# Performance work log

Hardware: AMD Instinct MI355X
Metric: run time of the kernel (lower is better)

The kernel has to match this reference:

```python
import jax, jax.numpy as jnp
import numpy as np
import math

B, T, D, H = 2, 2048, 1024, 16
DK = D // H
NEG = -1e9  # finite stand-in for -inf causal fill inside the ALiBi bias


def make_alibi_bias(n_heads: int, seq_len: int) -> jnp.ndarray:
    # standard ALiBi slopes: 2^(-8*h/H) for h = 1..H
    slopes = 2.0 ** (-8.0 * (np.arange(1, n_heads + 1) / n_heads))  # [H]
    pos = np.arange(seq_len)
    dist = pos[None, :] - pos[:, None]  # [T,T], j - i
    bias = slopes[:, None, None] * dist[None, :, :]  # [H,T,T], <=0 below diag
    bias = np.where(dist[None] > 0, NEG, bias)  # causal: mask future
    return jnp.asarray(bias, dtype=jnp.float32)


def setup_inputs() -> dict:
    key = jax.random.key(0)
    ks = jax.random.split(key, 8)
    s = 0.02
    return {
        "query": jax.random.normal(ks[0], (B, T, D), jnp.float32),
        "key": jax.random.normal(ks[1], (B, T, D), jnp.float32),
        "value": jax.random.normal(ks[2], (B, T, D), jnp.float32),
        "alibi_bias": make_alibi_bias(H, T),
        "wq": jax.random.normal(ks[3], (D, D), jnp.float32) * s,
        "wk": jax.random.normal(ks[4], (D, D), jnp.float32) * s,
        "wv": jax.random.normal(ks[5], (D, D), jnp.float32) * s,
        "wo": jax.random.normal(ks[6], (D, D), jnp.float32) * s,
        "bo": jnp.zeros((D,), jnp.float32),
    }


def reference(query, key, value, alibi_bias, wq, wk, wv, wo, bo):
    b, tq, d = query.shape
    # linear projections (torch Linear: x @ W^T), split heads -> [B,H,T,d_k]
    def split(x, w):
        y = jnp.einsum('btd,ed->bte', x, w)
        return y.reshape(b, -1, H, DK).transpose(0, 2, 1, 3)
    Q, K, V = split(query, wq), split(key, wk), split(value, wv)
    # scores + ALiBi bias (bias already encodes causality)
    scores = jnp.einsum('bhqd,bhkd->bhqk', Q, K) / math.sqrt(DK)
    scores = scores + alibi_bias[None]  # broadcast over batch
    attn = jax.nn.softmax(scores, axis=-1)
    out = jnp.einsum('bhqk,bhkd->bhqd', attn, V)  # [B,H,Tq,d_k]
    out = out.transpose(0, 2, 1, 3).reshape(b, tq, d)
    return jnp.einsum('btd,ed->bte', out, wo) + bo
```

## Files before the change

kernel.cpp:

```cpp
#include <hip/hip_runtime.h>
#include <hip/hip_bf16.h>
#include <stdint.h>

#define Bc   2
#define Tc   2048
#define Dc   1024
#define Hc   16
#define DKc  64
#define BTc  4096
#define LOG2E 1.44269504088896f

typedef unsigned short u16;
typedef unsigned int u32;
typedef __attribute__((ext_vector_type(8))) short bf16x8;
typedef __attribute__((ext_vector_type(4))) float f32x4;
typedef __attribute__((ext_vector_type(2))) u32 u32x2;

static __device__ __forceinline__ u16 f2bf(float f) {
  union { float f; unsigned u; } v; v.f = f;
  unsigned r = v.u + 0x7fffu + ((v.u >> 16) & 1u);
  return (u16)(r >> 16);
}

static __device__ __forceinline__ u32 cvt_pk_bf16(float lo, float hi) {
  u32 r;
  asm volatile("v_cvt_pk_bf16_f32 %0, %1, %2" : "=v"(r) : "v"(lo), "v"(hi));
  return r;
}

static __device__ __forceinline__ f32x4 mfma16(bf16x8 a, bf16x8 b, f32x4 c) {
  return __builtin_amdgcn_mfma_f32_16x16x32_bf16(a, b, c, 0, 0, 0);
}

__global__ void conv_kernel(const float* __restrict__ q, const float* __restrict__ k,
                            const float* __restrict__ v, const float* __restrict__ wq,
                            const float* __restrict__ wk, const float* __restrict__ wv,
                            const float* __restrict__ wo,
                            u16* __restrict__ Xq, u16* __restrict__ Xk, u16* __restrict__ Xv,
                            u16* __restrict__ Wq, u16* __restrict__ Wk, u16* __restrict__ Wv,
                            u16* __restrict__ Wo) {
  int z = blockIdx.z, bx = blockIdx.x;
  const float* src; u16* dst; int i;
  if (bx < 4096) {
    if (z == 3) return;
    src = z == 0 ? q : z == 1 ? k : v;
    dst = z == 0 ? Xq : z == 1 ? Xk : Xv;
    i = bx * 256 + threadIdx.x;
  } else {
    src = z == 0 ? wq : z == 1 ? wk : z == 2 ? wv : wo;
    dst = z == 0 ? Wq : z == 1 ? Wk : z == 2 ? Wv : Wo;
    i = (bx - 4096) * 256 + threadIdx.x;
  }
  float4 f = ((const float4*)src)[i];
  ushort4 r; r.x = f2bf(f.x); r.y = f2bf(f.y); r.z = f2bf(f.z); r.w = f2bf(f.w);
  ((ushort4*)dst)[i] = r;
}

#define AS1 const __attribute__((address_space(1))) void*
#define AS3 __attribute__((address_space(3))) void*

__global__ __launch_bounds__(256) void gemm_proj(const u16* __restrict__ Xq, const u16* __restrict__ Xk,
                                                 const u16* __restrict__ Xv, const u16* __restrict__ Wq,
                                                 const u16* __restrict__ Wk, const u16* __restrict__ Wv,
                                                 u16* __restrict__ Qh, u16* __restrict__ Kh,
                                                 u16* __restrict__ VTo) {
  __shared__ u16 As[128 * 32];
  __shared__ u16 Bs[128 * 32];
  int z = blockIdx.z;
  const u16* A = z == 0 ? Xq : z == 1 ? Xk : Xv;
  const u16* W = z == 0 ? Wq : z == 1 ? Wk : Wv;
  u16* outp    = z == 0 ? Qh : z == 1 ? Kh : VTo;
  float scale = (z == 0) ? 0.125f * LOG2E : 1.0f;
  int tid = threadIdx.x;
  int lane = tid & 63, wave = tid >> 6;
  int ln = lane & 15, g = lane >> 4;
  int m0 = blockIdx.x * 128, n0 = blockIdx.y * 128;
  int wm = (wave >> 1) * 64, wn = (wave & 1) * 64;
  f32x4 acc[4][4] = {};
  int c0 = tid, c1 = tid + 256;
  const u16* gA0 = A + (size_t)(m0 + (c0 >> 2)) * 1024 + (c0 & 3) * 8;
  const u16* gA1 = A + (size_t)(m0 + (c1 >> 2)) * 1024 + (c1 & 3) * 8;
  const u16* gW0 = W + (size_t)(n0 + (c0 >> 2)) * 1024 + (c0 & 3) * 8;
  const u16* gW1 = W + (size_t)(n0 + (c1 >> 2)) * 1024 + (c1 & 3) * 8;
  for (int k0 = 0; k0 < 1024; k0 += 32) {
    __builtin_amdgcn_global_load_lds((AS1)(gA0 + k0), (AS3)(As + c0 * 8), 16, 0, 0);
    __builtin_amdgcn_global_load_lds((AS1)(gA1 + k0), (AS3)(As + c1 * 8), 16, 0, 0);
    __builtin_amdgcn_global_load_lds((AS1)(gW0 + k0), (AS3)(Bs + c0 * 8), 16, 0, 0);
    __builtin_amdgcn_global_load_lds((AS1)(gW1 + k0), (AS3)(Bs + c1 * 8), 16, 0, 0);
    __syncthreads();
    bf16x8 af[4], bfr[4];
#pragma unroll
    for (int mi = 0; mi < 4; ++mi) af[mi]  = *(const bf16x8*)&As[(wm + mi * 16 + ln) * 32 + g * 8];
#pragma unroll
    for (int ni = 0; ni < 4; ++ni) bfr[ni] = *(const bf16x8*)&Bs[(wn + ni * 16 + ln) * 32 + g * 8];
#pragma unroll
    for (int mi = 0; mi < 4; ++mi)
#pragma unroll
      for (int ni = 0; ni < 4; ++ni)
        acc[mi][ni] = mfma16(af[mi], bfr[ni], acc[mi][ni]);
    __syncthreads();
  }
  if (z == 2) {
#pragma unroll
    for (int mi = 0; mi < 4; ++mi)
#pragma unroll
      for (int ni = 0; ni < 4; ++ni) {
        int t0 = m0 + wm + mi * 16 + g * 4;
        int gn = n0 + wn + ni * 16 + ln;
        size_t bhead = ((size_t)(t0 >> 11)) * Hc + (gn >> 6);
        ushort4 pk;
        pk.x = f2bf(acc[mi][ni][0]); pk.y = f2bf(acc[mi][ni][1]);
        pk.z = f2bf(acc[mi][ni][2]); pk.w = f2bf(acc[mi][ni][3]);
        *(ushort4*)&outp[(bhead * DKc + (gn & 63)) * Tc + (t0 & 2047)] = pk;
      }
  } else {
#pragma unroll
    for (int mi = 0; mi < 4; ++mi)
#pragma unroll
      for (int ni = 0; ni < 4; ++ni)
#pragma unroll
        for (int r = 0; r < 4; ++r) {
          int gm = m0 + wm + mi * 16 + g * 4 + r;
          int gn = n0 + wn + ni * 16 + ln;
          size_t bhead = ((size_t)(gm >> 11)) * Hc + (gn >> 6);
          outp[(bhead * Tc + (gm & 2047)) * DKc + (gn & 63)] = f2bf(acc[mi][ni][r] * scale);
        }
  }
}

__global__ __launch_bounds__(256) void gemm_out(const u16* __restrict__ Ain, const u16* __restrict__ W,
                                                float* __restrict__ of, const float* __restrict__ bias) {
  __shared__ u16 As[64 * 32];
  __shared__ u16 Bs[128 * 32];
  int tid = threadIdx.x;
  int lane = tid & 63, wave = tid >> 6;
  int ln = lane & 15, g = lane >> 4;
  int m0 = blockIdx.x * 64, n0 = blockIdx.y * 128;
  int wm = (wave >> 1) * 32, wn = (wave & 1) * 64;
  f32x4 acc[2][4] = {};
  int ca = tid, cb0 = tid, cb1 = tid + 256;
  const u16* gA  = Ain + (size_t)(m0 + (ca  >> 2)) * 1024 + (ca  & 3) * 8;
  const u16* gW0 = W   + (size_t)(n0 + (cb0 >> 2)) * 1024 + (cb0 & 3) * 8;
  const u16* gW1 = W   + (size_t)(n0 + (cb1 >> 2)) * 1024 + (cb1 & 3) * 8;
  for (int k0 = 0; k0 < 1024; k0 += 32) {
    __builtin_amdgcn_global_load_lds((AS1)(gA  + k0), (AS3)(As + ca  * 8), 16, 0, 0);
    __builtin_amdgcn_global_load_lds((AS1)(gW0 + k0), (AS3)(Bs + cb0 * 8), 16, 0, 0);
    __builtin_amdgcn_global_load_lds((AS1)(gW1 + k0), (AS3)(Bs + cb1 * 8), 16, 0, 0);
    __syncthreads();
    bf16x8 af[2], bfr[4];
#pragma unroll
    for (int mi = 0; mi < 2; ++mi) af[mi]  = *(const bf16x8*)&As[(wm + mi * 16 + ln) * 32 + g * 8];
#pragma unroll
    for (int ni = 0; ni < 4; ++ni) bfr[ni] = *(const bf16x8*)&Bs[(wn + ni * 16 + ln) * 32 + g * 8];
#pragma unroll
    for (int mi = 0; mi < 2; ++mi)
#pragma unroll
      for (int ni = 0; ni < 4; ++ni)
        acc[mi][ni] = mfma16(af[mi], bfr[ni], acc[mi][ni]);
    __syncthreads();
  }
#pragma unroll
  for (int mi = 0; mi < 2; ++mi)
#pragma unroll
    for (int ni = 0; ni < 4; ++ni)
#pragma unroll
      for (int r = 0; r < 4; ++r) {
        int gm = m0 + wm + mi * 16 + g * 4 + r;
        int gn = n0 + wn + ni * 16 + ln;
        of[(size_t)gm * 1024 + gn] = acc[mi][ni][r] + bias[gn];
      }
}

__global__ __launch_bounds__(256, 2) void flash_attn(const u16* __restrict__ Qh,
                                                     const u16* __restrict__ Kh,
                                                     const u16* __restrict__ VT,
                                                     u16* __restrict__ O) {
  __shared__ u16 Ks[2][64 * 64];
  __shared__ u16 Vs[2][64 * 64];
  __shared__ u16 P_lds[8][16][64];
  int d = blockIdx.x;
  int logical = (d & 7) * 64 + (d >> 3);
  int bh = logical >> 4, pid = logical & 15;
  int qhi = 16 + pid, qlo = 15 - pid;
  int b = bh >> 4, h = bh & (Hc - 1);
  int tid = threadIdx.x, wave = tid >> 6, lane = tid & 63;
  int ln = lane & 15, g = lane >> 4;
  float slope2 = exp2f(-0.5f * (float)(h + 1)) * LOG2E;

  const u16* gK = Kh + (size_t)bh * Tc * DKc;
  const u16* gV = VT + (size_t)bh * DKc * Tc;
  int c0 = tid, c1 = tid + 256;
  int r0 = c0 >> 3, r1 = c1 >> 3;
  int e0 = ((c0 & 7) << 3) ^ ((r0 & 7) << 3);
  int e1 = ((c1 & 7) << 3) ^ ((r1 & 7) << 3);
  size_t kO0 = (size_t)r0 * DKc + e0, kO1 = (size_t)r1 * DKc + e1;
  size_t vO0 = (size_t)r0 * Tc + e0, vO1 = (size_t)r1 * Tc + e1;

#define STAGE(bufi, ks_) do {                                                                  \
    __builtin_amdgcn_global_load_lds((AS1)(gK + (size_t)(ks_) * DKc + kO0),                    \
                                     (AS3)(&Ks[bufi][c0 * 8]), 16, 0, 0);                      \
    __builtin_amdgcn_global_load_lds((AS1)(gK + (size_t)(ks_) * DKc + kO1),                    \
                                     (AS3)(&Ks[bufi][c1 * 8]), 16, 0, 0);                      \
    __builtin_amdgcn_global_load_lds((AS1)(gV + (size_t)(ks_) + vO0),                          \
                                     (AS3)(&Vs[bufi][c0 * 8]), 16, 0, 0);                      \
    __builtin_amdgcn_global_load_lds((AS1)(gV + (size_t)(ks_) + vO1),                          \
                                     (AS3)(&Vs[bufi][c1 * 8]), 16, 0, 0);                      \
  } while (0)

  int qlocal = wave * 16 + ln;
  int qgH = qhi * 64 + qlocal, qgL = qlo * 64 + qlocal;
  const u16* QpH = Qh + ((size_t)bh * Tc + qgH) * DKc;
  const u16* QpL = Qh + ((size_t)bh * Tc + qgL) * DKc;
  bf16x8 qfH0 = *(const bf16x8*)&QpH[g * 8];
  bf16x8 qfH1 = *(const bf16x8*)&QpH[32 + g * 8];
  bf16x8 qfL0 = *(const bf16x8*)&QpL[g * 8];
  bf16x8 qfL1 = *(const bf16x8*)&QpL[32 + g * 8];

  float vb[4][4];
#pragma unroll
  for (int j = 0; j < 4; ++j)
#pragma unroll
    for (int r = 0; r < 4; ++r)
      vb[j][r] = slope2 * (float)(j * 16 + g * 4 + r);

  f32x4 accH[4] = {}, accL[4] = {};
  float MH = -1e30f, LH = 0.f, ML = -1e30f, LL = 0.f;

  auto tile_step = [&](int buf, int ks, bool diag, bf16x8 qf0, bf16x8 qf1,
                       int qg, float& Mx, float& Lx, f32x4* accO, int pslot) {
    f32x4 s[4] = {};
    __builtin_amdgcn_s_setprio(1);
#pragma unroll
    for (int j = 0; j < 4; ++j) {
      int row = j * 16 + ln, sw = (row & 7) << 3;
      bf16x8 kf0 = *(const bf16x8*)&Ks[buf][row * DKc + ((g * 8) ^ sw)];
      bf16x8 kf1 = *(const bf16x8*)&Ks[buf][row * DKc + ((32 + g * 8) ^ sw)];
      s[j] = mfma16(kf0, qf0, s[j]);
      s[j] = mfma16(kf1, qf1, s[j]);
    }
    __builtin_amdgcn_s_setprio(0);
    float vv[4][4];
    float mloc = -1e30f;
#pragma unroll
    for (int j = 0; j < 4; ++j)
#pragma unroll
      for (int r = 0; r < 4; ++r) {
        float t = s[j][r] + vb[j][r];
        if (diag) t = (j * 16 + g * 4 + r > qlocal) ? -1e30f : t;
        vv[j][r] = t;
        mloc = fmaxf(mloc, t);
      }
    mloc = fmaxf(mloc, __shfl_xor(mloc, 16, 64));
    mloc = fmaxf(mloc, __shfl_xor(mloc, 32, 64));
    float cterm = slope2 * (float)(ks - qg);
    float mc = mloc + cterm;
    if (__any(mc > Mx)) {
      float newM = fmaxf(Mx, mc);
      float sc = __builtin_amdgcn_exp2f(Mx - newM);
      Mx = newM;
      Lx *= sc;
      float scb[4];
#pragma unroll
      for (int r = 0; r < 4; ++r) scb[r] = __shfl(sc, g * 4 + r, 64);
#pragma unroll
      for (int nd = 0; nd < 4; ++nd)
#pragma unroll
        for (int r = 0; r < 4; ++r) accO[nd][r] *= scb[r];
    }
    float dsub = Mx - cterm;
    float rs = 0.f;
#pragma unroll
    for (int j = 0; j < 4; ++j)
#pragma unroll
      for (int r = 0; r < 4; ++r) {
        float p = __builtin_amdgcn_exp2f(vv[j][r] - dsub);
        vv[j][r] = p;
        rs += p;
      }
    Lx += rs;
    char* Prow = (char*)&P_lds[pslot][ln][0];
    int psw = (ln & 7) << 4;
#pragma unroll
    for (int j = 0; j < 4; ++j) {
      u32x2 w;
      w.x = cvt_pk_bf16(vv[j][0], vv[j][1]);
      w.y = cvt_pk_bf16(vv[j][2], vv[j][3]);
      *(u32x2*)(Prow + ((j * 32 + g * 8) ^ psw)) = w;
    }
    __builtin_amdgcn_s_setprio(1);
#pragma unroll
    for (int kk = 0; kk < 2; ++kk) {
      bf16x8 pa = *(const bf16x8*)(Prow + ((kk * 64 + g * 16) ^ psw));
#pragma unroll
      for (int nd = 0; nd < 4; ++nd) {
        int d2 = nd * 16 + ln, o = kk * 32 + g * 8;
        bf16x8 vf = *(const bf16x8*)&Vs[buf][d2 * DKc + (o ^ ((d2 & 7) << 3))];
        accO[nd] = mfma16(pa, vf, accO[nd]);
      }
    }
    __builtin_amdgcn_s_setprio(0);
  };

  STAGE(0, qhi * 64);
  __syncthreads();
  int buf = 0;
  for (int kb = qhi; kb >= 0; --kb) {
    int ks = kb * 64;
    if (kb > 0) STAGE(buf ^ 1, ks - 64);
    tile_step(buf, ks, kb == qhi, qfH0, qfH1, qgH, MH, LH, accH, wave);
    if (kb <= qlo)
      tile_step(buf, ks, kb == qlo, qfL0, qfL1, qgL, ML, LL, accL, wave + 4);
    __syncthreads();
    buf ^= 1;
  }

#pragma unroll
  for (int tile = 0; tile < 2; ++tile) {
    float Lx = tile ? LL : LH;
    f32x4* accO = tile ? accL : accH;
    int qb = tile ? qlo : qhi;
    float Lf = Lx + __shfl_xor(Lx, 16, 64);
    Lf = Lf + __shfl_xor(Lf, 32, 64);
    float linv[4];
#pragma unroll
    for (int r = 0; r < 4; ++r) linv[r] = 1.0f / __shfl(Lf, g * 4 + r, 64);
#pragma unroll
    for (int nd = 0; nd < 4; ++nd)
#pragma unroll
      for (int r = 0; r < 4; ++r) {
        int t = qb * 64 + wave * 16 + g * 4 + r;
        int dcol = h * 64 + nd * 16 + ln;
        O[((size_t)(b * Tc + t)) * Dc + dcol] = f2bf(accO[nd][r] * linv[r]);
      }
  }
#undef STAGE
}

extern "C" void kernel_launch(void* const* d_in, const int* in_sizes, int n_in,
                              void* d_out, int out_size, void* d_ws, size_t ws_size,
                              hipStream_t stream) {
  const float* q  = (const float*)d_in[0];
  const float* k  = (const float*)d_in[1];
  const float* v  = (const float*)d_in[2];
  const float* wq = (const float*)d_in[4];
  const float* wk = (const float*)d_in[5];
  const float* wv = (const float*)d_in[6];
  const float* wo = (const float*)d_in[7];
  const float* bo = (const float*)d_in[8];

  char* ws = (char*)d_ws;
  const size_t MB = 1024 * 1024;
  u16* Xq = (u16*)(ws + 0 * MB);
  u16* Xk = (u16*)(ws + 8 * MB);
  u16* Xv = (u16*)(ws + 16 * MB);
  u16* Wq = (u16*)(ws + 24 * MB);
  u16* Wk = (u16*)(ws + 26 * MB);
  u16* Wv = (u16*)(ws + 28 * MB);
  u16* Wo = (u16*)(ws + 30 * MB);
  u16* Qh = (u16*)(ws + 32 * MB);
  u16* Kh = (u16*)(ws + 40 * MB);
  u16* VT = (u16*)(ws + 48 * MB);
  u16* Ob = (u16*)(ws + 56 * MB);
  float* out = (float*)d_out;

  conv_kernel<<<dim3(4096 + 1024, 1, 4), 256, 0, stream>>>(q, k, v, wq, wk, wv, wo,
                                                           Xq, Xk, Xv, Wq, Wk, Wv, Wo);
  gemm_proj<<<dim3(32, 8, 3), 256, 0, stream>>>(Xq, Xk, Xv, Wq, Wk, Wv, Qh, Kh, VT);
  flash_attn<<<dim3(512), 256, 0, stream>>>(Qh, Kh, VT, Ob);
  gemm_out<<<dim3(64, 8), 256, 0, stream>>>(Ob, Wo, out, bo);
}
```

Baseline: 128.4 us.

## Double-buffer LDS tiles in projection and output GEMMs

Both the QKV projection GEMM and the output projection GEMM now use two LDS buffers. The global-to-LDS load for the next K-slice is issued before the MFMAs on the current slice, which removes one barrier per iteration and overlaps memory latency with compute. LDS use per block doubles, which may lower occupancy. The global_load_lds writes could still be in flight when the barrier is reached, so correctness depends on the compiler inserting vmcnt waits before __syncthreads.

```diff
diff --git a/kernel.cpp b/kernel.cpp
--- a/kernel.cpp
+++ b/kernel.cpp
@@ -64,8 +64,8 @@
                                                  const u16* __restrict__ Wk, const u16* __restrict__ Wv,
                                                  u16* __restrict__ Qh, u16* __restrict__ Kh,
                                                  u16* __restrict__ VTo) {
-  __shared__ u16 As[128 * 32];
-  __shared__ u16 Bs[128 * 32];
+  __shared__ u16 As[2][128 * 32];
+  __shared__ u16 Bs[2][128 * 32];
   int z = blockIdx.z;
   const u16* A = z == 0 ? Xq : z == 1 ? Xk : Xv;
   const u16* W = z == 0 ? Wq : z == 1 ? Wk : Wv;
@@ -82,24 +82,34 @@
   const u16* gA1 = A + (size_t)(m0 + (c1 >> 2)) * 1024 + (c1 & 3) * 8;
   const u16* gW0 = W + (size_t)(n0 + (c0 >> 2)) * 1024 + (c0 & 3) * 8;
   const u16* gW1 = W + (size_t)(n0 + (c1 >> 2)) * 1024 + (c1 & 3) * 8;
-  for (int k0 = 0; k0 < 1024; k0 += 32) {
-    __builtin_amdgcn_global_load_lds((AS1)(gA0 + k0), (AS3)(As + c0 * 8), 16, 0, 0);
-    __builtin_amdgcn_global_load_lds((AS1)(gA1 + k0), (AS3)(As + c1 * 8), 16, 0, 0);
-    __builtin_amdgcn_global_load_lds((AS1)(gW0 + k0), (AS3)(Bs + c0 * 8), 16, 0, 0);
-    __builtin_amdgcn_global_load_lds((AS1)(gW1 + k0), (AS3)(Bs + c1 * 8), 16, 0, 0);
-    __syncthreads();
+
+#define PSTAGE(bufi, k0_) do {                                                                 \
+    __builtin_amdgcn_global_load_lds((AS1)(gA0 + (k0_)), (AS3)(&As[bufi][c0 * 8]), 16, 0, 0);  \
+    __builtin_amdgcn_global_load_lds((AS1)(gA1 + (k0_)), (AS3)(&As[bufi][c1 * 8]), 16, 0, 0);  \
+    __builtin_amdgcn_global_load_lds((AS1)(gW0 + (k0_)), (AS3)(&Bs[bufi][c0 * 8]), 16, 0, 0);  \
+    __builtin_amdgcn_global_load_lds((AS1)(gW1 + (k0_)), (AS3)(&Bs[bufi][c1 * 8]), 16, 0, 0);  \
+  } while (0)
+
+  PSTAGE(0, 0);
+  __syncthreads();
+  int cur = 0;
+  for (int it = 0; it < 32; ++it) {
+    if (it < 31) PSTAGE(cur ^ 1, (it + 1) * 32);
     bf16x8 af[4], bfr[4];
 #pragma unroll
-    for (int mi = 0; mi < 4; ++mi) af[mi]  = *(const bf16x8*)&As[(wm + mi * 16 + ln) * 32 + g * 8];
-#pragma unroll
-    for (int ni = 0; ni < 4; ++ni) bfr[ni] = *(const bf16x8*)&Bs[(wn + ni * 16 + ln) * 32 + g * 8];
+    for (int mi = 0; mi < 4; ++mi) af[mi]  = *(const bf16x8*)&As[cur][(wm + mi * 16 + ln) * 32 + g * 8];
+#pragma unroll
+    for (int ni = 0; ni < 4; ++ni) bfr[ni] = *(const bf16x8*)&Bs[cur][(wn + ni * 16 + ln) * 32 + g * 8];
 #pragma unroll
     for (int mi = 0; mi < 4; ++mi)
 #pragma unroll
       for (int ni = 0; ni < 4; ++ni)
         acc[mi][ni] = mfma16(af[mi], bfr[ni], acc[mi][ni]);
     __syncthreads();
-  }
+    cur ^= 1;
+  }
+#undef PSTAGE
+
   if (z == 2) {
 #pragma unroll
     for (int mi = 0; mi < 4; ++mi)
@@ -130,8 +140,8 @@
 
 __global__ __launch_bounds__(256) void gemm_out(const u16* __restrict__ Ain, const u16* __restrict__ W,
                                                 float* __restrict__ of, const float* __restrict__ bias) {
-  __shared__ u16 As[64 * 32];
-  __shared__ u16 Bs[128 * 32];
+  __shared__ u16 As[2][64 * 32];
+  __shared__ u16 Bs[2][128 * 32];
   int tid = threadIdx.x;
   int lane = tid & 63, wave = tid >> 6;
   int ln = lane & 15, g = lane >> 4;
@@ -142,23 +152,33 @@
   const u16* gA  = Ain + (size_t)(m0 + (ca  >> 2)) * 1024 + (ca  & 3) * 8;
   const u16* gW0 = W   + (size_t)(n0 + (cb0 >> 2)) * 1024 + (cb0 & 3) * 8;
   const u16* gW1 = W   + (size_t)(n0 + (cb1 >> 2)) * 1024 + (cb1 & 3) * 8;
-  for (int k0 = 0; k0 < 1024; k0 += 32) {
-    __builtin_amdgcn_global_load_lds((AS1)(gA  + k0), (AS3)(As + ca  * 8), 16, 0, 0);
-    __builtin_amdgcn_global_load_lds((AS1)(gW0 + k0), (AS3)(Bs + cb0 * 8), 16, 0, 0);
-    __builtin_amdgcn_global_load_lds((AS1)(gW1 + k0), (AS3)(Bs + cb1 * 8), 16, 0, 0);
-    __syncthreads();
+
+#define OSTAGE(bufi, k0_) do {                                                                 \
+    __builtin_amdgcn_global_load_lds((AS1)(gA  + (k0_)), (AS3)(&As[bufi][ca  * 8]), 16, 0, 0); \
+    __builtin_amdgcn_global_load_lds((AS1)(gW0 + (k0_)), (AS3)(&Bs[bufi][cb0 * 8]), 16, 0, 0); \
+    __builtin_amdgcn_global_load_lds((AS1)(gW1 + (k0_)), (AS3)(&Bs[bufi][cb1 * 8]), 16, 0, 0); \
+  } while (0)
+
+  OSTAGE(0, 0);
+  __syncthreads();
+  int cur = 0;
+  for (int it = 0; it < 32; ++it) {
+    if (it < 31) OSTAGE(cur ^ 1, (it + 1) * 32);
     bf16x8 af[2], bfr[4];
 #pragma unroll
-    for (int mi = 0; mi < 2; ++mi) af[mi]  = *(const bf16x8*)&As[(wm + mi * 16 + ln) * 32 + g * 8];
-#pragma unroll
-    for (int ni = 0; ni < 4; ++ni) bfr[ni] = *(const bf16x8*)&Bs[(wn + ni * 16 + ln) * 32 + g * 8];
+    for (int mi = 0; mi < 2; ++mi) af[mi]  = *(const bf16x8*)&As[cur][(wm + mi * 16 + ln) * 32 + g * 8];
+#pragma unroll
+    for (int ni = 0; ni < 4; ++ni) bfr[ni] = *(const bf16x8*)&Bs[cur][(wn + ni * 16 + ln) * 32 + g * 8];
 #pragma unroll
     for (int mi = 0; mi < 2; ++mi)
 #pragma unroll
       for (int ni = 0; ni < 4; ++ni)
         acc[mi][ni] = mfma16(af[mi], bfr[ni], acc[mi][ni]);
     __syncthreads();
-  }
+    cur ^= 1;
+  }
+#undef OSTAGE
+
 #pragma unroll
   for (int mi = 0; mi < 2; ++mi)
 #pragma unroll
```

Measured after the change: 118.9 us. -7.3%, faster.
